# Optimization experiments

Hardware: AMD Instinct MI355X
Metric: run time of the kernel (lower is better)

## Reference

```python
import jax, jax.numpy as jnp
import numpy as np

TEMP = 0.07
POS_MARGIN = 0.1
NEG_MARGIN = 0.1
B, PM, PH, NM, NH, D = 512, 8, 16, 64, 64, 2048


def _l2(x):
    # torch F.cosine_similarity clamps norms at 1e-8
    return x / jnp.maximum(jnp.linalg.norm(x, axis=-1, keepdims=True), 1e-8)


def setup_inputs() -> dict:
    key = jax.random.key(0)
    k0, k1, k2, k3, k4 = jax.random.split(key, 5)
    return {
        "query_embeds": jax.random.normal(k0, (B, D), jnp.float32),
        "pos_main": jax.random.normal(k1, (B, PM, D), jnp.float32),
        "pos_hard": jax.random.normal(k2, (B, PH, D), jnp.float32),
        "neg_main": jax.random.normal(k3, (B, NM, D), jnp.float32),
        "neg_hard": jax.random.normal(k4, (B, NH, D), jnp.float32),
    }


def reference(query_embeds, pos_main, pos_hard, neg_main, neg_hard):
    q = _l2(query_embeds)            # [B, D]
    pm = _l2(pos_main)               # [B, PM, D]
    ph = _l2(pos_hard)               # [B, PH, D]
    nm = _l2(neg_main)               # [B, NM, D]
    nh = _l2(neg_hard)               # [B, NH, D]

    pm_sims = jnp.einsum('bd,bpd->bp', q, pm)      # [B, PM]
    anchor = pm_sims[:, 0]                          # pos_main_sims[0] per sample

    pos_score = jnp.exp(pm_sims / TEMP).sum(axis=1)
    ph_sims = jnp.einsum('bd,bpd->bp', q, ph)
    p_mask = (ph_sims >= anchor[:, None] - POS_MARGIN).astype(q.dtype)
    pos_score = pos_score + jnp.sum(p_mask * jnp.exp(ph_sims / TEMP), axis=1)

    thr = anchor[:, None] + NEG_MARGIN              # [B, 1] broadcastable threshold

    nm_sims = jnp.einsum('bd,bnd->bn', q, nm)
    neg_score = jnp.sum((nm_sims <= thr).astype(q.dtype) * jnp.exp(nm_sims / TEMP), axis=1)
    nh_sims = jnp.einsum('bd,bnd->bn', q, nh)
    neg_score = neg_score + jnp.sum((nh_sims <= thr).astype(q.dtype) * jnp.exp(nh_sims / TEMP), axis=1)

    off = 1.0 - jnp.eye(B, dtype=q.dtype)           # j != i mask

    # query_i vs query_j
    qq = q @ q.T                                    # [B, B]
    neg_score = neg_score + jnp.sum(off * (qq <= thr).astype(q.dtype) * jnp.exp(qq / TEMP), axis=1)

    pf = pm[:, 0]                                   # first positive of each sample, normalized [B, D]
    # curr_pos_i vs other_pos_j
    pp = pf @ pf.T
    neg_score = neg_score + jnp.sum(off * (pp <= thr).astype(q.dtype) * jnp.exp(pp / TEMP), axis=1)
    # query_i vs other_pos_j
    qp = q @ pf.T
    neg_score = neg_score + jnp.sum(off * (qp <= thr).astype(q.dtype) * jnp.exp(qp / TEMP), axis=1)

    loss = -jnp.log(pos_score / (pos_score + neg_score + 1e-8))
    return loss.mean()
```

## Files before the change

kernel.cpp:

```cpp
#include <hip/hip_runtime.h>
#include <math.h>

#define NB   512
#define NPM  8
#define NPH  16
#define NNM  64
#define NNH  64
#define ND   2048
#define TEMP_INV 14.285714285714285714f
#define POSM 0.1f
#define NEGM 0.1f

static constexpr int ROWS_PER_B = NPM + NPH + NNM + NNH;
static constexpr int WPB        = 16;

typedef __attribute__((ext_vector_type(8))) short bf16x8;
typedef __attribute__((ext_vector_type(4))) float f32x4;

__device__ __forceinline__ unsigned short f2bf(float f) {
  unsigned int u = __float_as_uint(f);
  return (unsigned short)((u + 0x7FFFu + ((u >> 16) & 1u)) >> 16);
}

__device__ __forceinline__ void acc_ss_dot(const float4 v, const float4 u,
                                           float& ss, float& dot) {
  ss  = fmaf(v.x, v.x, ss);  ss  = fmaf(v.y, v.y, ss);
  ss  = fmaf(v.z, v.z, ss);  ss  = fmaf(v.w, v.w, ss);
  dot = fmaf(v.x, u.x, dot); dot = fmaf(v.y, u.y, dot);
  dot = fmaf(v.z, u.z, dot); dot = fmaf(v.w, u.w, dot);
}

__device__ __forceinline__ void block_reduce2(float& a, float& b) {
#pragma unroll
  for (int off = 32; off > 0; off >>= 1) {
    a += __shfl_down(a, off);
    b += __shfl_down(b, off);
  }
  __shared__ float sa[4], sb[4];
  const int w = threadIdx.x >> 6;
  if ((threadIdx.x & 63) == 0) { sa[w] = a; sb[w] = b; }
  __syncthreads();
  a = sa[0] + sa[1] + sa[2] + sa[3];
  b = sb[0] + sb[1] + sb[2] + sb[3];
  __syncthreads();
}

__global__ __launch_bounds__(256) void k_prep(const float* __restrict__ q,
                                              const float* __restrict__ pm,
                                              float* __restrict__ qn,
                                              unsigned short* __restrict__ qb,
                                              unsigned short* __restrict__ pb,
                                              float* __restrict__ anchor,
                                              float* __restrict__ pos,
                                              float* __restrict__ neg) {
  const int b = blockIdx.x;
  const int t = threadIdx.x;

  const float4* qrow = (const float4*)(q + (size_t)b * ND);
  float4 q0 = qrow[t];
  float4 q1 = qrow[t + 256];
  float ss = 0.f, dummy = 0.f;
  ss = fmaf(q0.x, q0.x, ss); ss = fmaf(q0.y, q0.y, ss);
  ss = fmaf(q0.z, q0.z, ss); ss = fmaf(q0.w, q0.w, ss);
  ss = fmaf(q1.x, q1.x, ss); ss = fmaf(q1.y, q1.y, ss);
  ss = fmaf(q1.z, q1.z, ss); ss = fmaf(q1.w, q1.w, ss);
  block_reduce2(ss, dummy);
  const float qinv = 1.0f / fmaxf(sqrtf(ss), 1e-8f);
  q0.x *= qinv; q0.y *= qinv; q0.z *= qinv; q0.w *= qinv;
  q1.x *= qinv; q1.y *= qinv; q1.z *= qinv; q1.w *= qinv;
  float4* qno = (float4*)(qn + (size_t)b * ND);
  qno[t] = q0; qno[t + 256] = q1;
  ushort4* qbo = (ushort4*)(qb + (size_t)b * ND);
  ushort4 qc0, qc1;
  qc0.x = f2bf(q0.x); qc0.y = f2bf(q0.y); qc0.z = f2bf(q0.z); qc0.w = f2bf(q0.w);
  qc1.x = f2bf(q1.x); qc1.y = f2bf(q1.y); qc1.z = f2bf(q1.z); qc1.w = f2bf(q1.w);
  qbo[t] = qc0; qbo[t + 256] = qc1;

  const float4* prow = (const float4*)(pm + (size_t)b * NPM * ND);
  float4 p0 = prow[t];
  float4 p1 = prow[t + 256];
  float pss = 0.f, dot = 0.f;
  acc_ss_dot(p0, q0, pss, dot);
  acc_ss_dot(p1, q1, pss, dot);
  block_reduce2(pss, dot);
  const float pinv = 1.0f / fmaxf(sqrtf(pss), 1e-8f);
  p0.x *= pinv; p0.y *= pinv; p0.z *= pinv; p0.w *= pinv;
  p1.x *= pinv; p1.y *= pinv; p1.z *= pinv; p1.w *= pinv;
  ushort4* pbo = (ushort4*)(pb + (size_t)b * ND);
  ushort4 pc0, pc1;
  pc0.x = f2bf(p0.x); pc0.y = f2bf(p0.y); pc0.z = f2bf(p0.z); pc0.w = f2bf(p0.w);
  pc1.x = f2bf(p1.x); pc1.y = f2bf(p1.y); pc1.z = f2bf(p1.z); pc1.w = f2bf(p1.w);
  pbo[t] = pc0; pbo[t + 256] = pc1;

  if (t == 0) {
    anchor[b] = dot * pinv;
    pos[b] = 0.f;
    neg[b] = 0.f;
  }
}

__global__ __launch_bounds__(256) void k_rows(const float* __restrict__ pmain,
                                              const float* __restrict__ phard,
                                              const float* __restrict__ nmain,
                                              const float* __restrict__ nhard,
                                              const float* __restrict__ qn,
                                              const float* __restrict__ anchor,
                                              float* __restrict__ pos,
                                              float* __restrict__ neg) {
  const int wgl    = blockIdx.x * 4 + (threadIdx.x >> 6);
  const int lane   = threadIdx.x & 63;
  const int b      = wgl >> 4;
  const int wslice = wgl & 15;

  auto rowp = [&](int r) -> const float4* {
    const float* p;
    if (r < NPM)                 p = pmain + ((size_t)b * NPM + r) * ND;
    else if (r < NPM + NPH)      p = phard + ((size_t)b * NPH + (r - NPM)) * ND;
    else if (r < NPM + NPH + NNM) p = nmain + ((size_t)b * NNM + (r - NPM - NPH)) * ND;
    else                          p = nhard + ((size_t)b * NNH + (r - NPM - NPH - NNM)) * ND;
    return (const float4*)p;
  };

  const float4* qrow = (const float4*)(qn + (size_t)b * ND);
  float4 u[8];
#pragma unroll
  for (int j = 0; j < 8; j++) u[j] = qrow[lane + 64 * j];
  const float anc = anchor[b];

  float pacc = 0.f, nacc = 0.f;
  const int n = (ROWS_PER_B - wslice + WPB - 1) / WPB;

  float4 va[8], vb[8];
  {
    const float4* p0 = rowp(wslice);
#pragma unroll
    for (int j = 0; j < 8; j++) va[j] = p0[lane + 64 * j];
  }

  auto body = [&](float4 (&vcur)[8], float4 (&vnext)[8], int i) {
    const int rn = wslice + WPB * (i + 1);
    const float4* pn = rowp(rn < ROWS_PER_B ? rn : wslice);
#pragma unroll
    for (int j = 0; j < 8; j++) vnext[j] = pn[lane + 64 * j];
    __builtin_amdgcn_sched_barrier(0);

    float ss = 0.f, dot = 0.f;
#pragma unroll
    for (int j = 0; j < 8; j++) acc_ss_dot(vcur[j], u[j], ss, dot);
#pragma unroll
    for (int off = 32; off > 0; off >>= 1) {
      ss  += __shfl_xor(ss, off);
      dot += __shfl_xor(dot, off);
    }
    const float sim = dot / fmaxf(sqrtf(ss), 1e-8f);
    const float e   = expf(sim * TEMP_INV);
    const int   r   = wslice + WPB * i;
    if (r < NPM) {
      pacc += e;
    } else if (r < NPM + NPH) {
      if (sim >= anc - POSM) pacc += e;
    } else {
      if (sim <= anc + NEGM) nacc += e;
    }
  };

  int i = 0;
  for (; i + 2 <= n; i += 2) {
    body(va, vb, i);
    body(vb, va, i + 1);
  }
  if (i < n) body(va, vb, i);

  if (lane == 0) {
    if (pacc != 0.f) atomicAdd(pos + b, pacc);
    if (nacc != 0.f) atomicAdd(neg + b, nacc);
  }
}

__global__ __launch_bounds__(256) void k_sim(const unsigned short* __restrict__ qb,
                                             const unsigned short* __restrict__ pb,
                                             const float* __restrict__ anchor,
                                             float* __restrict__ neg) {
  const int z = blockIdx.z;
  const unsigned short* __restrict__ A = (z == 1) ? pb : qb;
  const unsigned short* __restrict__ B = (z == 0) ? qb : pb;

  const int wid  = blockIdx.x * 4 + (threadIdx.x >> 6);
  const int m    = wid >> 4;
  const int n2   = wid & 15;
  const int lane = threadIdx.x & 63;
  const int r16  = lane & 15;
  const int kc   = lane >> 4;

  const size_t abase  = ((size_t)(m * 16 + r16)) * ND + kc * 8;
  const size_t b0base = ((size_t)(n2 * 32 + r16)) * ND + kc * 8;
  const size_t b1base = b0base + (size_t)16 * ND;

  f32x4 acc0 = {0.f, 0.f, 0.f, 0.f};
  f32x4 acc1 = {0.f, 0.f, 0.f, 0.f};
#pragma unroll 2
  for (int k0 = 0; k0 < ND; k0 += 64) {
    const bf16x8 a0  = *(const bf16x8*)(A + abase  + k0);
    const bf16x8 a1  = *(const bf16x8*)(A + abase  + k0 + 32);
    const bf16x8 b00 = *(const bf16x8*)(B + b0base + k0);
    const bf16x8 b10 = *(const bf16x8*)(B + b1base + k0);
    const bf16x8 b01 = *(const bf16x8*)(B + b0base + k0 + 32);
    const bf16x8 b11 = *(const bf16x8*)(B + b1base + k0 + 32);
    acc0 = __builtin_amdgcn_mfma_f32_16x16x32_bf16(a0, b00, acc0, 0, 0, 0);
    acc1 = __builtin_amdgcn_mfma_f32_16x16x32_bf16(a0, b10, acc1, 0, 0, 0);
    acc0 = __builtin_amdgcn_mfma_f32_16x16x32_bf16(a1, b01, acc0, 0, 0, 0);
    acc1 = __builtin_amdgcn_mfma_f32_16x16x32_bf16(a1, b11, acc1, 0, 0, 0);
  }

  const int rbase = m * 16 + kc * 4;
  const int gc0   = n2 * 32 + r16;
#pragma unroll
  for (int j = 0; j < 4; j++) {
    const int gr = rbase + j;
    const float thr = anchor[gr] + NEGM;
    float s = 0.f;
    const float v0 = acc0[j];
    const float v1 = acc1[j];
    if (gr != gc0      && v0 <= thr) s += expf(v0 * TEMP_INV);
    if (gr != gc0 + 16 && v1 <= thr) s += expf(v1 * TEMP_INV);
    s += __shfl_xor(s, 1);
    s += __shfl_xor(s, 2);
    s += __shfl_xor(s, 4);
    s += __shfl_xor(s, 8);
    if (r16 == 0) atomicAdd(neg + gr, s);
  }
}

__global__ __launch_bounds__(512) void k_loss(const float* __restrict__ pos,
                                              const float* __restrict__ neg,
                                              float* __restrict__ out) {
  const int t = threadIdx.x;
  const float p = pos[t];
  const float n = neg[t];
  float l = -logf(p / (p + n + 1e-8f));
#pragma unroll
  for (int off = 32; off > 0; off >>= 1) l += __shfl_down(l, off);
  __shared__ float s[8];
  if ((t & 63) == 0) s[t >> 6] = l;
  __syncthreads();
  if (t == 0) {
    float tot = 0.f;
#pragma unroll
    for (int i = 0; i < 8; i++) tot += s[i];
    out[0] = tot / (float)NB;
  }
}

extern "C" void kernel_launch(void* const* d_in, const int* in_sizes, int n_in,
                              void* d_out, int out_size, void* d_ws, size_t ws_size,
                              hipStream_t stream) {
  const float* q  = (const float*)d_in[0];
  const float* pm = (const float*)d_in[1];
  const float* ph = (const float*)d_in[2];
  const float* nm = (const float*)d_in[3];
  const float* nh = (const float*)d_in[4];
  float* out = (float*)d_out;

  float* ws = (float*)d_ws;
  float*          qn     = ws;
  unsigned short* qb     = (unsigned short*)(ws + (size_t)NB * ND);
  unsigned short* pb     = qb + (size_t)NB * ND;
  float*          anchor = (float*)(pb + (size_t)NB * ND);
  float*          pos    = anchor + NB;
  float*          neg    = pos + NB;

  k_prep<<<NB, 256, 0, stream>>>(q, pm, qn, qb, pb, anchor, pos, neg);
  k_rows<<<(NB * WPB) / 4, 256, 0, stream>>>(pm, ph, nm, nh, qn, anchor, pos, neg);
  k_sim<<<dim3(128, 1, 3), 256, 0, stream>>>(qb, pb, anchor, neg);
  k_loss<<<1, 512, 0, stream>>>(pos, neg, out);
}
```

Measured before the change: 192.9 us.

## Stream row loads through LDS with async global_load_lds double buffering

The row-similarity kernel now stages each 8KB row into a per-wave LDS double buffer using direct global-to-LDS loads, waiting on vmcnt before consuming the current buffer. This replaces the register prefetch. Waves per batch drop from 16 to 8, so each wave handles more rows, and the loop becomes a fixed count. It also switches to rsqrt and the fast exp. The goal is to keep more bytes in flight per wave while freeing registers. The costs are 64KB of LDS per block, which limits occupancy, and slightly different numerics from the fast math.

New measurement: 171.4 us. 11.1% less time.

```diff
diff --git a/kernel.cpp b/kernel.cpp
--- a/kernel.cpp
+++ b/kernel.cpp
@@ -12,7 +12,8 @@
 #define NEGM 0.1f
 
 static constexpr int ROWS_PER_B = NPM + NPH + NNM + NNH;
-static constexpr int WPB        = 16;
+static constexpr int WPB        = 8;
+static constexpr int NRW        = ROWS_PER_B / WPB;
 
 typedef __attribute__((ext_vector_type(8))) short bf16x8;
 typedef __attribute__((ext_vector_type(4))) float f32x4;
@@ -43,6 +44,12 @@
   a = sa[0] + sa[1] + sa[2] + sa[3];
   b = sb[0] + sb[1] + sb[2] + sb[3];
   __syncthreads();
+}
+
+__device__ __forceinline__ void gl_lds16(const float* g, float* l) {
+  __builtin_amdgcn_global_load_lds(
+      (const __attribute__((address_space(1))) unsigned int*)g,
+      (__attribute__((address_space(3))) unsigned int*)l, 16, 0, 0);
 }
 
 __global__ __launch_bounds__(256) void k_prep(const float* __restrict__ q,
@@ -107,18 +114,27 @@
                                               const float* __restrict__ anchor,
                                               float* __restrict__ pos,
                                               float* __restrict__ neg) {
-  const int wgl    = blockIdx.x * 4 + (threadIdx.x >> 6);
+  __shared__ float lds[4][2][ND];
+
+  const int wid    = threadIdx.x >> 6;
   const int lane   = threadIdx.x & 63;
-  const int b      = wgl >> 4;
-  const int wslice = wgl & 15;
-
-  auto rowp = [&](int r) -> const float4* {
+  const int wgl    = blockIdx.x * 4 + wid;
+  const int b      = wgl >> 3;
+  const int wslice = wgl & 7;
+
+  auto rowp = [&](int k) -> const float* {
+    const int r = wslice + WPB * k;
     const float* p;
-    if (r < NPM)                 p = pmain + ((size_t)b * NPM + r) * ND;
-    else if (r < NPM + NPH)      p = phard + ((size_t)b * NPH + (r - NPM)) * ND;
+    if (r < NPM)                  p = pmain + ((size_t)b * NPM + r) * ND;
+    else if (r < NPM + NPH)       p = phard + ((size_t)b * NPH + (r - NPM)) * ND;
     else if (r < NPM + NPH + NNM) p = nmain + ((size_t)b * NNM + (r - NPM - NPH)) * ND;
     else                          p = nhard + ((size_t)b * NNH + (r - NPM - NPH - NNM)) * ND;
-    return (const float4*)p;
+    return p + lane * 4;
+  };
+
+  auto stage = [&](int k, float* slot) {
+#pragma unroll
+    for (int c = 0; c < 8; c++) gl_lds16(rowp(k) + c * 256, slot + c * 256);
   };
 
   const float4* qrow = (const float4*)(qn + (size_t)b * ND);
@@ -128,33 +144,26 @@
   const float anc = anchor[b];
 
   float pacc = 0.f, nacc = 0.f;
-  const int n = (ROWS_PER_B - wslice + WPB - 1) / WPB;
-
-  float4 va[8], vb[8];
-  {
-    const float4* p0 = rowp(wslice);
-#pragma unroll
-    for (int j = 0; j < 8; j++) va[j] = p0[lane + 64 * j];
-  }
-
-  auto body = [&](float4 (&vcur)[8], float4 (&vnext)[8], int i) {
-    const int rn = wslice + WPB * (i + 1);
-    const float4* pn = rowp(rn < ROWS_PER_B ? rn : wslice);
-#pragma unroll
-    for (int j = 0; j < 8; j++) vnext[j] = pn[lane + 64 * j];
-    __builtin_amdgcn_sched_barrier(0);
-
-    float ss = 0.f, dot = 0.f;
-#pragma unroll
-    for (int j = 0; j < 8; j++) acc_ss_dot(vcur[j], u[j], ss, dot);
+
+  auto process = [&](const float* slot, int k) {
+    const float4* lb = (const float4*)slot;
+    float ss0 = 0.f, ss1 = 0.f, d0 = 0.f, d1 = 0.f;
+#pragma unroll
+    for (int j = 0; j < 8; j += 2) {
+      const float4 v0 = lb[lane + 64 * j];
+      const float4 v1 = lb[lane + 64 * (j + 1)];
+      acc_ss_dot(v0, u[j], ss0, d0);
+      acc_ss_dot(v1, u[j + 1], ss1, d1);
+    }
+    float ss = ss0 + ss1, dt = d0 + d1;
 #pragma unroll
     for (int off = 32; off > 0; off >>= 1) {
-      ss  += __shfl_xor(ss, off);
-      dot += __shfl_xor(dot, off);
+      ss += __shfl_xor(ss, off);
+      dt += __shfl_xor(dt, off);
     }
-    const float sim = dot / fmaxf(sqrtf(ss), 1e-8f);
-    const float e   = expf(sim * TEMP_INV);
-    const int   r   = wslice + WPB * i;
+    const float sim = dt * rsqrtf(fmaxf(ss, 1e-16f));
+    const float e   = __expf(sim * TEMP_INV);
+    const int   r   = wslice + WPB * k;
     if (r < NPM) {
       pacc += e;
     } else if (r < NPM + NPH) {
@@ -164,12 +173,20 @@
     }
   };
 
-  int i = 0;
-  for (; i + 2 <= n; i += 2) {
-    body(va, vb, i);
-    body(vb, va, i + 1);
-  }
-  if (i < n) body(va, vb, i);
+  float* cur = &lds[wid][0][0];
+  float* nxt = &lds[wid][1][0];
+
+  stage(0, cur);
+  for (int k = 0; k + 1 < NRW; ++k) {
+    stage(k + 1, nxt);
+    asm volatile("s_waitcnt vmcnt(8)" ::: "memory");
+    __builtin_amdgcn_sched_barrier(0);
+    process(cur, k);
+    float* t = cur; cur = nxt; nxt = t;
+  }
+  asm volatile("s_waitcnt vmcnt(0)" ::: "memory");
+  __builtin_amdgcn_sched_barrier(0);
+  process(cur, NRW - 1);
 
   if (lane == 0) {
     if (pacc != 0.f) atomicAdd(pos + b, pacc);
```
